# Kernel tuning notes

Measured on AMD Instinct MI355X. Metric: run time of the kernel, lower is better.

Reference implementation:

```python
import jax, jax.numpy as jnp
import numpy as np

VOCAB_SIZE = 148
START_IDX = 1
LATENT = 32
HID = 256
NUM_LAYERS = 2
B = 8192
T = 50


def setup_inputs() -> dict:
    key = jax.random.key(0)
    ks = jax.random.split(key, 20)
    s = 0.05
    inp = {
        "z": jax.random.normal(ks[0], (B, LATENT), jnp.float32),
        "target_tokens": jax.random.randint(ks[1], (B, T), 0, VOCAB_SIZE),
        "emb": jax.random.normal(ks[2], (VOCAB_SIZE, HID), jnp.float32) * s,
        "W_lat": jax.random.normal(ks[3], (HID * NUM_LAYERS, LATENT), jnp.float32) * s,
        "b_lat": jnp.zeros((HID * NUM_LAYERS,), jnp.float32),
        "W_ih0": jax.random.normal(ks[4], (3 * HID, HID), jnp.float32) * s,
        "W_hh0": jax.random.normal(ks[5], (3 * HID, HID), jnp.float32) * s,
        "b_ih0": jnp.zeros((3 * HID,), jnp.float32),
        "b_hh0": jnp.zeros((3 * HID,), jnp.float32),
        "W_ih1": jax.random.normal(ks[6], (3 * HID, HID), jnp.float32) * s,
        "W_hh1": jax.random.normal(ks[7], (3 * HID, HID), jnp.float32) * s,
        "b_ih1": jnp.zeros((3 * HID,), jnp.float32),
        "b_hh1": jnp.zeros((3 * HID,), jnp.float32),
        "W1": jax.random.normal(ks[8], (HID, HID), jnp.float32) * s,
        "b1": jnp.zeros((HID,), jnp.float32),
        "W2": jax.random.normal(ks[9], (VOCAB_SIZE, HID), jnp.float32) * s,
        "b2": jnp.zeros((VOCAB_SIZE,), jnp.float32),
    }
    # padding_idx=0 row of embedding is zero in torch
    inp["emb"] = inp["emb"].at[0].set(0.0)
    return inp


def _gru_cell(x, h, W_ih, W_hh, b_ih, b_hh):
    # PyTorch GRUCell math
    gi = x @ W_ih.T + b_ih          # [B, 3H]
    gh = h @ W_hh.T + b_hh          # [B, 3H]
    i_r, i_z, i_n = jnp.split(gi, 3, axis=-1)
    h_r, h_z, h_n = jnp.split(gh, 3, axis=-1)
    r = jax.nn.sigmoid(i_r + h_r)
    zg = jax.nn.sigmoid(i_z + h_z)
    n = jnp.tanh(i_n + r * h_n)
    return (1.0 - zg) * n + zg * h


def reference(z, target_tokens, emb, W_lat, b_lat,
              W_ih0, W_hh0, b_ih0, b_hh0,
              W_ih1, W_hh1, b_ih1, b_hh1,
              W1, b1, W2, b2):
    batch = z.shape[0]
    # init hidden: (B, L*H) -> (L, B, H)
    h = (z @ W_lat.T + b_lat).reshape(batch, NUM_LAYERS, HID).transpose(1, 0, 2)
    # teacher forcing ratio 1.0: inputs = [START, tgt[:,1], ..., tgt[:,T-2]]
    start = jnp.full((batch, 1), START_IDX, dtype=target_tokens.dtype)
    tokens_in = jnp.concatenate([start, target_tokens[:, 1:T - 1]], axis=1)  # [B, T-1]
    x = emb[tokens_in]                       # [B, T-1, H]
    xs = x.transpose(1, 0, 2)                # [T-1, B, H]

    def step(carry, x_t):
        h0, h1 = carry
        h0n = _gru_cell(x_t, h0, W_ih0, W_hh0, b_ih0, b_hh0)
        h1n = _gru_cell(h0n, h1, W_ih1, W_hh1, b_ih1, b_hh1)
        return (h0n, h1n), h1n

    _, ys = jax.lax.scan(step, (h[0], h[1]), xs)   # ys: [T-1, B, H]
    y = ys.transpose(1, 0, 2)                      # [B, T-1, H]
    hdd = jax.nn.relu(jnp.einsum('bth,oh->bto', y, W1) + b1)
    logits = jnp.einsum('bth,vh->btv', hdd, W2) + b2   # [B, T-1, V]
    generated = target_tokens[:, 1:]                   # pure teacher forcing
    return logits, generated
```

## Files before the change

kernel.cpp:

```cpp
#include <hip/hip_runtime.h>
#include <hip/hip_bf16.h>
#include <math.h>


#define BATCH 8192
#define TTOT 50
#define TS 49
#define HID 256
#define N3 768
#define VOCAB 148
#define START_TOK 1
#define HPAD 264

typedef short bf16x8 __attribute__((ext_vector_type(8)));
typedef float f32x4 __attribute__((ext_vector_type(4)));

constexpr size_t OFF_Y    = 0;
constexpr size_t OFF_WH0B = OFF_Y + 205520896;
constexpr size_t OFF_WI1B = OFF_WH0B + 393216;
constexpr size_t OFF_WH1B = OFF_WI1B + 393216;
constexpr size_t OFF_W1B  = OFF_WH1B + 393216;
constexpr size_t OFF_W2B  = OFF_W1B + 131072;
constexpr size_t OFF_TAB  = OFF_W2B + 81920;
constexpr size_t OFF_H0F  = OFF_TAB + 454656;
constexpr size_t OFF_H1F  = OFF_H0F + 8388608;

__device__ __forceinline__ short f2b(float f) {
    union { float f; unsigned int u; } v; v.f = f;
    unsigned int u = v.u;
    return (short)((u + 0x7FFFu + ((u >> 16) & 1u)) >> 16);
}
__device__ __forceinline__ float sigm(float x) {
    x = fminf(fmaxf(x, -30.f), 30.f);
    return 1.f / (1.f + __expf(-x));
}
__device__ __forceinline__ float tanh_(float x) {
    x = fminf(fmaxf(x, -15.f), 15.f);
    float e = __expf(-2.f * x);
    return (1.f - e) / (1.f + e);
}

__global__ __launch_bounds__(256) void convert_w(
    const float* __restrict__ Wh0, const float* __restrict__ Wi1, const float* __restrict__ Wh1,
    const float* __restrict__ W1, const float* __restrict__ W2,
    short* __restrict__ Wh0b, short* __restrict__ Wi1b, short* __restrict__ Wh1b,
    short* __restrict__ W1b, short* __restrict__ W2b)
{
    int tid = blockIdx.x * 256 + threadIdx.x;
    const int WSZ = N3 * HID;
    const float* S; short* D; int n; bool pad148 = false;
    if (tid < WSZ) { S = Wh0; D = Wh0b; n = tid; }
    else if (tid < 2 * WSZ) { S = Wi1; D = Wi1b; n = tid - WSZ; }
    else if (tid < 3 * WSZ) { S = Wh1; D = Wh1b; n = tid - 2 * WSZ; }
    else if (tid < 3 * WSZ + 65536) { S = W1; D = W1b; n = tid - 3 * WSZ; }
    else if (tid < 3 * WSZ + 65536 + 40960) { S = W2; D = W2b; n = tid - 3 * WSZ - 65536; pad148 = true; }
    else return;
    int e = n & 7, lane = (n >> 3) & 63, kc = (n >> 9) & 7, nt = n >> 12;
    int row = nt * 16 + (lane & 15);
    int k = kc * 32 + (lane >> 4) * 8 + e;
    float v = (pad148 && row >= VOCAB) ? 0.f : S[row * HID + k];
    D[n] = f2b(v);
}

__global__ __launch_bounds__(256) void build_tab(
    const float* __restrict__ emb, const float* __restrict__ Wih0,
    const float* __restrict__ bih0, float* __restrict__ tab)
{
    int o = blockIdx.x * 256 + threadIdx.x;
    if (o >= VOCAB * N3) return;
    int v = o / N3, c = o - v * N3;
    const float* er = emb + v * HID;
    const float* wr = Wih0 + c * HID;
    float s = bih0[c];
    #pragma unroll 8
    for (int k = 0; k < HID; ++k) s += er[k] * wr[k];
    tab[o] = s;
}

__global__ __launch_bounds__(256) void init_h(
    const float* __restrict__ z, const float* __restrict__ Wl, const float* __restrict__ bl,
    float* __restrict__ h0f, float* __restrict__ h1f)
{
    int tid = blockIdx.x * 256 + threadIdx.x;
    int b = tid >> 9, o = tid & 511;
    const float* zr = z + b * 32;
    const float* wr = Wl + o * 32;
    float s = bl[o];
    #pragma unroll
    for (int k = 0; k < 32; ++k) s += zr[k] * wr[k];
    if (o < HID) h0f[b * HID + o] = s;
    else         h1f[b * HID + o - HID] = s;
}

__global__ __launch_bounds__(512, 2) void gru_persistent(
    const int* __restrict__ toks, const float* __restrict__ tab,
    const short* __restrict__ Wh0, const short* __restrict__ Wi1, const short* __restrict__ Wh1,
    const float* __restrict__ bhh0, const float* __restrict__ bih1, const float* __restrict__ bhh1,
    const float* __restrict__ h0f, const float* __restrict__ h1f,
    short* __restrict__ Yb)
{
    __shared__ short h0L[32 * HPAD];
    __shared__ short h1L[32 * HPAD];
    __shared__ int tokL[32 * TTOT];

    const int tid = threadIdx.x;
    const int wave = tid >> 6, lane = tid & 63, quad = lane >> 4, l15 = lane & 15;
    const int rowbase = blockIdx.x * 32;

    for (int idx = tid; idx < 1024; idx += 512) {
        int row = idx >> 5, col = (idx & 31) * 8;
        const float* s0 = h0f + (size_t)(rowbase + row) * HID + col;
        const float* s1 = h1f + (size_t)(rowbase + row) * HID + col;
        short t0[8], t1[8];
        #pragma unroll
        for (int j = 0; j < 8; ++j) { t0[j] = f2b(s0[j]); t1[j] = f2b(s1[j]); }
        *(bf16x8*)&h0L[row * HPAD + col] = *(bf16x8*)t0;
        *(bf16x8*)&h1L[row * HPAD + col] = *(bf16x8*)t1;
    }
    for (int idx = tid; idx < 32 * TTOT; idx += 512) {
        int row = idx / TTOT, tt = idx - row * TTOT;
        tokL[idx] = (tt == 0) ? START_TOK : toks[(size_t)(rowbase + row) * TTOT + tt];
    }

    float h0r[2][2][4], h1r[2][2][4];
    #pragma unroll
    for (int i = 0; i < 2; ++i)
        #pragma unroll
        for (int c = 0; c < 2; ++c) {
            int col = wave * 32 + c * 16 + l15;
            #pragma unroll
            for (int r_ = 0; r_ < 4; ++r_) {
                int row = rowbase + 16 * i + quad * 4 + r_;
                h0r[i][c][r_] = h0f[(size_t)row * HID + col];
                h1r[i][c][r_] = h1f[(size_t)row * HID + col];
            }
        }
    __syncthreads();

    const short* WA[6]; const short* WB[6]; const short* WC[6];
    #pragma unroll
    for (int g = 0; g < 3; ++g)
        #pragma unroll
        for (int c = 0; c < 2; ++c) {
            int nt = g * 16 + wave * 2 + c;
            WA[g * 2 + c] = Wh0 + (size_t)nt * 4096 + lane * 8;
            WB[g * 2 + c] = Wh1 + (size_t)nt * 4096 + lane * 8;
            WC[g * 2 + c] = Wi1 + (size_t)nt * 4096 + lane * 8;
        }

    const size_t mtg0 = (size_t)(rowbase >> 4);

    for (int t = 0; t < TS; ++t) {
        f32x4 acc0[2][6] = {};
        f32x4 accrz[2][4] = {}, acchn[2][2] = {};
        #pragma unroll 2
        for (int kc = 0; kc < 8; ++kc) {
            bf16x8 a0[2], a1[2];
            #pragma unroll
            for (int i = 0; i < 2; ++i) {
                a0[i] = *(const bf16x8*)&h0L[(16 * i + l15) * HPAD + kc * 32 + quad * 8];
                a1[i] = *(const bf16x8*)&h1L[(16 * i + l15) * HPAD + kc * 32 + quad * 8];
            }
            #pragma unroll
            for (int j = 0; j < 6; ++j) {
                bf16x8 b0 = *(const bf16x8*)(WA[j] + kc * 512);
                #pragma unroll
                for (int i = 0; i < 2; ++i)
                    acc0[i][j] = __builtin_amdgcn_mfma_f32_16x16x32_bf16(a0[i], b0, acc0[i][j], 0, 0, 0);
            }
            #pragma unroll
            for (int j = 0; j < 6; ++j) {
                bf16x8 b1 = *(const bf16x8*)(WB[j] + kc * 512);
                #pragma unroll
                for (int i = 0; i < 2; ++i) {
                    if (j < 4) accrz[i][j] = __builtin_amdgcn_mfma_f32_16x16x32_bf16(a1[i], b1, accrz[i][j], 0, 0, 0);
                    else       acchn[i][j - 4] = __builtin_amdgcn_mfma_f32_16x16x32_bf16(a1[i], b1, acchn[i][j - 4], 0, 0, 0);
                }
            }
        }
        #pragma unroll
        for (int c = 0; c < 2; ++c) {
            int col = wave * 32 + c * 16 + l15;
            float br = bhh0[col], bz = bhh0[256 + col], bn = bhh0[512 + col];
            #pragma unroll
            for (int i = 0; i < 2; ++i)
                #pragma unroll
                for (int r_ = 0; r_ < 4; ++r_) {
                    int rl = 16 * i + quad * 4 + r_;
                    const float* tp = tab + (size_t)tokL[rl * TTOT + t] * N3 + col;
                    float r  = sigm(acc0[i][c][r_] + br + tp[0]);
                    float z  = sigm(acc0[i][2 + c][r_] + bz + tp[256]);
                    float n  = tanh_(tp[512] + r * (acc0[i][4 + c][r_] + bn));
                    h0r[i][c][r_] = (1.f - z) * n + z * h0r[i][c][r_];
                }
        }
        __syncthreads();
        #pragma unroll
        for (int c = 0; c < 2; ++c) {
            int col = wave * 32 + c * 16 + l15;
            #pragma unroll
            for (int i = 0; i < 2; ++i)
                #pragma unroll
                for (int r_ = 0; r_ < 4; ++r_)
                    h0L[(16 * i + quad * 4 + r_) * HPAD + col] = f2b(h0r[i][c][r_]);
        }
        __syncthreads();

        f32x4 accgn[2][2] = {};
        #pragma unroll 2
        for (int kc = 0; kc < 8; ++kc) {
            bf16x8 a[2];
            #pragma unroll
            for (int i = 0; i < 2; ++i)
                a[i] = *(const bf16x8*)&h0L[(16 * i + l15) * HPAD + kc * 32 + quad * 8];
            #pragma unroll
            for (int j = 0; j < 6; ++j) {
                bf16x8 b = *(const bf16x8*)(WC[j] + kc * 512);
                #pragma unroll
                for (int i = 0; i < 2; ++i) {
                    if (j < 4) accrz[i][j] = __builtin_amdgcn_mfma_f32_16x16x32_bf16(a[i], b, accrz[i][j], 0, 0, 0);
                    else       accgn[i][j - 4] = __builtin_amdgcn_mfma_f32_16x16x32_bf16(a[i], b, accgn[i][j - 4], 0, 0, 0);
                }
            }
        }
        #pragma unroll
        for (int c = 0; c < 2; ++c) {
            int col = wave * 32 + c * 16 + l15;
            float brr = bih1[col] + bhh1[col];
            float brz = bih1[256 + col] + bhh1[256 + col];
            float bni = bih1[512 + col], bnh = bhh1[512 + col];
            #pragma unroll
            for (int i = 0; i < 2; ++i)
                #pragma unroll
                for (int r_ = 0; r_ < 4; ++r_) {
                    float r = sigm(accrz[i][c][r_] + brr);
                    float z = sigm(accrz[i][2 + c][r_] + brz);
                    float n = tanh_(accgn[i][c][r_] + bni + r * (acchn[i][c][r_] + bnh));
                    h1r[i][c][r_] = (1.f - z) * n + z * h1r[i][c][r_];
                }
        }
        __syncthreads();
        #pragma unroll
        for (int c = 0; c < 2; ++c) {
            int col = wave * 32 + c * 16 + l15;
            #pragma unroll
            for (int i = 0; i < 2; ++i)
                #pragma unroll
                for (int r_ = 0; r_ < 4; ++r_)
                    h1L[(16 * i + quad * 4 + r_) * HPAD + col] = f2b(h1r[i][c][r_]);
        }
        __syncthreads();

        #pragma unroll
        for (int it = 0; it < 2; ++it) {
            int pair = wave + it * 8;
            int mt = pair >> 3, kc = pair & 7;
            bf16x8 v = *(const bf16x8*)&h1L[(mt * 16 + l15) * HPAD + kc * 32 + quad * 8];
            *(bf16x8*)(Yb + ((((size_t)t * 512 + mtg0 + mt) * 8 + kc) << 9) + lane * 8) = v;
        }
    }
}

__global__ __launch_bounds__(256) void head_kernel(
    const short* __restrict__ YP, const short* __restrict__ W1P, const float* __restrict__ b1,
    const short* __restrict__ W2P, const float* __restrict__ b2, float* __restrict__ out)
{
    __shared__ short hddL[64 * HPAD];
    int wave = threadIdx.x >> 6;
    int lane = threadIdx.x & 63;
    int quad = lane >> 4;
    int l15  = lane & 15;
    int rbase = blockIdx.x * 64;
    int tt = rbase >> 13;
    int mb = (rbase & 8191) >> 4;

    {
        const short* ybase = YP + ((size_t)tt * 512 + mb) * 4096 + lane * 8;
        const short* wbase = W1P + (size_t)(wave * 4) * 4096 + lane * 8;
        f32x4 acc[4][4] = {};
        #pragma unroll 2
        for (int kc = 0; kc < 8; ++kc) {
            bf16x8 a[4], bfr[4];
            #pragma unroll
            for (int i = 0; i < 4; ++i) a[i] = *(const bf16x8*)(ybase + (size_t)i * 4096 + kc * 512);
            #pragma unroll
            for (int j = 0; j < 4; ++j) bfr[j] = *(const bf16x8*)(wbase + (size_t)j * 4096 + kc * 512);
            #pragma unroll
            for (int i = 0; i < 4; ++i)
                #pragma unroll
                for (int j = 0; j < 4; ++j)
                    acc[i][j] = __builtin_amdgcn_mfma_f32_16x16x32_bf16(a[i], bfr[j], acc[i][j], 0, 0, 0);
        }
        #pragma unroll
        for (int i = 0; i < 4; ++i)
            #pragma unroll
            for (int j = 0; j < 4; ++j)
                #pragma unroll
                for (int r = 0; r < 4; ++r) {
                    int rl = i * 16 + quad * 4 + r;
                    int c  = wave * 64 + j * 16 + l15;
                    float v = acc[i][j][r] + b1[c];
                    hddL[rl * HPAD + c] = f2b(fmaxf(v, 0.f));
                }
    }
    __syncthreads();
    for (int s = wave * 5; s < wave * 5 + 5; ++s) {
        int ct = s >> 1, rh = s & 1;
        const short* w2b = W2P + (size_t)ct * 4096 + lane * 8;
        f32x4 acc2[2] = {};
        #pragma unroll 2
        for (int kc = 0; kc < 8; ++kc) {
            bf16x8 bfr = *(const bf16x8*)(w2b + kc * 512);
            #pragma unroll
            for (int it = 0; it < 2; ++it) {
                bf16x8 a = *(const bf16x8*)&hddL[(rh * 32 + it * 16 + l15) * HPAD + kc * 32 + quad * 8];
                acc2[it] = __builtin_amdgcn_mfma_f32_16x16x32_bf16(a, bfr, acc2[it], 0, 0, 0);
            }
        }
        int col = ct * 16 + l15;
        if (col < VOCAB) {
            #pragma unroll
            for (int it = 0; it < 2; ++it)
                #pragma unroll
                for (int r = 0; r < 4; ++r) {
                    int rl = rh * 32 + it * 16 + quad * 4 + r;
                    int gr = rbase + rl;
                    int t2 = gr >> 13;
                    int bb = gr & 8191;
                    out[((size_t)bb * TS + t2) * VOCAB + col] = acc2[it][r] + b2[col];
                }
        }
    }
}

__global__ __launch_bounds__(256) void gen_copy(const int* __restrict__ toks, float* __restrict__ out2)
{
    int tid = blockIdx.x * 256 + threadIdx.x;
    if (tid < BATCH * TS) {
        int b = tid / TS, j = tid - b * TS;
        out2[tid] = (float)toks[b * TTOT + j + 1];
    }
}

extern "C" void kernel_launch(void* const* d_in, const int* in_sizes, int n_in,
                              void* d_out, int out_size, void* d_ws, size_t ws_size,
                              hipStream_t stream) {
    const float* z     = (const float*)d_in[0];
    const int*   toks  = (const int*)d_in[1];
    const float* emb   = (const float*)d_in[2];
    const float* W_lat = (const float*)d_in[3];
    const float* b_lat = (const float*)d_in[4];
    const float* W_ih0 = (const float*)d_in[5];
    const float* W_hh0 = (const float*)d_in[6];
    const float* b_ih0 = (const float*)d_in[7];
    const float* b_hh0 = (const float*)d_in[8];
    const float* W_ih1 = (const float*)d_in[9];
    const float* W_hh1 = (const float*)d_in[10];
    const float* b_ih1 = (const float*)d_in[11];
    const float* b_hh1 = (const float*)d_in[12];
    const float* W1    = (const float*)d_in[13];
    const float* b1    = (const float*)d_in[14];
    const float* W2    = (const float*)d_in[15];
    const float* b2    = (const float*)d_in[16];

    char* w = (char*)d_ws;
    short* Yb   = (short*)(w + OFF_Y);
    short* Wh0b = (short*)(w + OFF_WH0B);
    short* Wi1b = (short*)(w + OFF_WI1B);
    short* Wh1b = (short*)(w + OFF_WH1B);
    short* W1b  = (short*)(w + OFF_W1B);
    short* W2b  = (short*)(w + OFF_W2B);
    float* tab  = (float*)(w + OFF_TAB);
    float* h0f  = (float*)(w + OFF_H0F);
    float* h1f  = (float*)(w + OFF_H1F);

    float* out_logits = (float*)d_out;
    float* out_gen    = out_logits + (size_t)BATCH * TS * VOCAB;

    convert_w<<<2720, 256, 0, stream>>>(W_hh0, W_ih1, W_hh1, W1, W2,
                                        Wh0b, Wi1b, Wh1b, W1b, W2b);
    build_tab<<<(VOCAB * N3 + 255) / 256, 256, 0, stream>>>(emb, W_ih0, b_ih0, tab);
    init_h<<<(BATCH * 512) / 256, 256, 0, stream>>>(z, W_lat, b_lat, h0f, h1f);
    gen_copy<<<(BATCH * TS + 255) / 256, 256, 0, stream>>>(toks, out_gen);

    gru_persistent<<<256, 512, 0, stream>>>(toks, tab, Wh0b, Wi1b, Wh1b,
                                            b_hh0, b_ih1, b_hh1, h0f, h1f, Yb);

    head_kernel<<<(BATCH * TS) / 64, 256, 0, stream>>>(Yb, W1b, b1, W2b, b2, out_logits);
}
```

Measured before the change: 1.440 ms.

## Halve GRU rows per block, double grid, fold biases into split input tables

The persistent GRU kernel now gives each block 16 batch rows instead of 32 and launches 512 blocks with higher occupancy bounds, so more blocks and CUs share the serial recurrence. The layer-0 input table is split into an interleaved r/z table, with the hidden biases folded in, and a separate n table, so the gate loads are paired float2 reads. Biases are hoisted out of the time loop, sigmoid clamps are removed, and bf16 packing uses v_cvt_pk_bf16_f32. Trade-off: each block reuses every weight fragment it loads across half as many rows, so total weight traffic from L2 roughly doubles.

```diff
diff --git a/kernel.cpp b/kernel.cpp
--- a/kernel.cpp
+++ b/kernel.cpp
@@ -22,6 +22,7 @@
 constexpr size_t OFF_W1B  = OFF_WH1B + 393216;
 constexpr size_t OFF_W2B  = OFF_W1B + 131072;
 constexpr size_t OFF_TAB  = OFF_W2B + 81920;
+constexpr size_t OFF_TABN = OFF_TAB + 303104;
 constexpr size_t OFF_H0F  = OFF_TAB + 454656;
 constexpr size_t OFF_H1F  = OFF_H0F + 8388608;
 
@@ -31,11 +32,10 @@
     return (short)((u + 0x7FFFu + ((u >> 16) & 1u)) >> 16);
 }
 __device__ __forceinline__ float sigm(float x) {
-    x = fminf(fmaxf(x, -30.f), 30.f);
     return 1.f / (1.f + __expf(-x));
 }
 __device__ __forceinline__ float tanh_(float x) {
-    x = fminf(fmaxf(x, -15.f), 15.f);
+    x = fmaxf(x, -15.f);
     float e = __expf(-2.f * x);
     return (1.f - e) / (1.f + e);
 }
@@ -62,19 +62,23 @@
     D[n] = f2b(v);
 }
 
-__global__ __launch_bounds__(256) void build_tab(
+__global__ __launch_bounds__(256) void build_tab2(
     const float* __restrict__ emb, const float* __restrict__ Wih0,
-    const float* __restrict__ bih0, float* __restrict__ tab)
+    const float* __restrict__ bih0, const float* __restrict__ bhh0,
+    float* __restrict__ tab_rz, float* __restrict__ tab_n)
 {
     int o = blockIdx.x * 256 + threadIdx.x;
     if (o >= VOCAB * N3) return;
-    int v = o / N3, c = o - v * N3;
+    int v = o / N3, cc = o - v * N3;
+    int g = cc >> 8, c = cc & 255;
     const float* er = emb + v * HID;
-    const float* wr = Wih0 + c * HID;
-    float s = bih0[c];
+    const float* wr = Wih0 + cc * HID;
+    float s = bih0[cc];
     #pragma unroll 8
     for (int k = 0; k < HID; ++k) s += er[k] * wr[k];
-    tab[o] = s;
+    if (g == 0)      tab_rz[(((v << 8) + c) << 1) + 0] = s + bhh0[c];
+    else if (g == 1) tab_rz[(((v << 8) + c) << 1) + 1] = s + bhh0[256 + c];
+    else             tab_n[(v << 8) + c] = s;
 }
 
 __global__ __launch_bounds__(256) void init_h(
@@ -92,23 +96,24 @@
     else         h1f[b * HID + o - HID] = s;
 }
 
-__global__ __launch_bounds__(512, 2) void gru_persistent(
-    const int* __restrict__ toks, const float* __restrict__ tab,
+__global__ __launch_bounds__(512, 4) void gru_persistent(
+    const int* __restrict__ toks,
+    const float* __restrict__ tab_rz, const float* __restrict__ tab_n,
     const short* __restrict__ Wh0, const short* __restrict__ Wi1, const short* __restrict__ Wh1,
     const float* __restrict__ bhh0, const float* __restrict__ bih1, const float* __restrict__ bhh1,
     const float* __restrict__ h0f, const float* __restrict__ h1f,
     short* __restrict__ Yb)
 {
-    __shared__ short h0L[32 * HPAD];
-    __shared__ short h1L[32 * HPAD];
-    __shared__ int tokL[32 * TTOT];
+    __shared__ short h0L[16 * HPAD];
+    __shared__ short h1L[16 * HPAD];
+    __shared__ int tokL[16 * TTOT];
 
     const int tid = threadIdx.x;
     const int wave = tid >> 6, lane = tid & 63, quad = lane >> 4, l15 = lane & 15;
-    const int rowbase = blockIdx.x * 32;
-
-    for (int idx = tid; idx < 1024; idx += 512) {
-        int row = idx >> 5, col = (idx & 31) * 8;
+    const int rowbase = blockIdx.x * 16;
+
+    {
+        int row = tid >> 5, col = (tid & 31) * 8;
         const float* s0 = h0f + (size_t)(rowbase + row) * HID + col;
         const float* s1 = h1f + (size_t)(rowbase + row) * HID + col;
         short t0[8], t1[8];
@@ -117,147 +122,131 @@
         *(bf16x8*)&h0L[row * HPAD + col] = *(bf16x8*)t0;
         *(bf16x8*)&h1L[row * HPAD + col] = *(bf16x8*)t1;
     }
-    for (int idx = tid; idx < 32 * TTOT; idx += 512) {
+    for (int idx = tid; idx < 16 * TTOT; idx += 512) {
         int row = idx / TTOT, tt = idx - row * TTOT;
         tokL[idx] = (tt == 0) ? START_TOK : toks[(size_t)(rowbase + row) * TTOT + tt];
     }
 
-    float h0r[2][2][4], h1r[2][2][4];
-    #pragma unroll
-    for (int i = 0; i < 2; ++i)
-        #pragma unroll
-        for (int c = 0; c < 2; ++c) {
-            int col = wave * 32 + c * 16 + l15;
-            #pragma unroll
-            for (int r_ = 0; r_ < 4; ++r_) {
-                int row = rowbase + 16 * i + quad * 4 + r_;
-                h0r[i][c][r_] = h0f[(size_t)row * HID + col];
-                h1r[i][c][r_] = h1f[(size_t)row * HID + col];
-            }
-        }
+    int colc[2]; colc[0] = wave * 32 + l15; colc[1] = colc[0] + 16;
+    float h0r[2][4], h1r[2][4];
+    #pragma unroll
+    for (int c = 0; c < 2; ++c)
+        #pragma unroll
+        for (int r_ = 0; r_ < 4; ++r_) {
+            int row = rowbase + quad * 4 + r_;
+            h0r[c][r_] = h0f[(size_t)row * HID + colc[c]];
+            h1r[c][r_] = h1f[(size_t)row * HID + colc[c]];
+        }
+
+    float bn0[2], brr[2], brz[2], bni[2], bnh[2];
+    #pragma unroll
+    for (int c = 0; c < 2; ++c) {
+        int col = colc[c];
+        bn0[c] = bhh0[512 + col];
+        brr[c] = bih1[col] + bhh1[col];
+        brz[c] = bih1[256 + col] + bhh1[256 + col];
+        bni[c] = bih1[512 + col];
+        bnh[c] = bhh1[512 + col];
+    }
+
+    int woff[6];
+    #pragma unroll
+    for (int g = 0; g < 3; ++g)
+        #pragma unroll
+        for (int c = 0; c < 2; ++c)
+            woff[g * 2 + c] = ((g * 16 + wave * 2 + c) << 12) + lane * 8;
+
+    const int a0base = l15 * HPAD + quad * 8;
+    const int hwbase = (quad * 4) * HPAD + colc[0];
+    int tokrow[4];
+    #pragma unroll
+    for (int r_ = 0; r_ < 4; ++r_) tokrow[r_] = (quad * 4 + r_) * TTOT;
+    short* yptr = Yb + ((((size_t)blockIdx.x << 3) + wave) << 9) + lane * 8;
+
     __syncthreads();
 
-    const short* WA[6]; const short* WB[6]; const short* WC[6];
-    #pragma unroll
-    for (int g = 0; g < 3; ++g)
-        #pragma unroll
-        for (int c = 0; c < 2; ++c) {
-            int nt = g * 16 + wave * 2 + c;
-            WA[g * 2 + c] = Wh0 + (size_t)nt * 4096 + lane * 8;
-            WB[g * 2 + c] = Wh1 + (size_t)nt * 4096 + lane * 8;
-            WC[g * 2 + c] = Wi1 + (size_t)nt * 4096 + lane * 8;
-        }
-
-    const size_t mtg0 = (size_t)(rowbase >> 4);
-
     for (int t = 0; t < TS; ++t) {
-        f32x4 acc0[2][6] = {};
-        f32x4 accrz[2][4] = {}, acchn[2][2] = {};
+        f32x4 acc0[6] = {};
+        f32x4 accrz[4] = {}, acchn[2] = {};
         #pragma unroll 2
         for (int kc = 0; kc < 8; ++kc) {
-            bf16x8 a0[2], a1[2];
-            #pragma unroll
-            for (int i = 0; i < 2; ++i) {
-                a0[i] = *(const bf16x8*)&h0L[(16 * i + l15) * HPAD + kc * 32 + quad * 8];
-                a1[i] = *(const bf16x8*)&h1L[(16 * i + l15) * HPAD + kc * 32 + quad * 8];
-            }
+            bf16x8 a0 = *(const bf16x8*)&h0L[a0base + kc * 32];
+            bf16x8 a1 = *(const bf16x8*)&h1L[a0base + kc * 32];
             #pragma unroll
             for (int j = 0; j < 6; ++j) {
-                bf16x8 b0 = *(const bf16x8*)(WA[j] + kc * 512);
-                #pragma unroll
-                for (int i = 0; i < 2; ++i)
-                    acc0[i][j] = __builtin_amdgcn_mfma_f32_16x16x32_bf16(a0[i], b0, acc0[i][j], 0, 0, 0);
+                bf16x8 b0 = *(const bf16x8*)(Wh0 + woff[j] + kc * 512);
+                acc0[j] = __builtin_amdgcn_mfma_f32_16x16x32_bf16(a0, b0, acc0[j], 0, 0, 0);
             }
             #pragma unroll
             for (int j = 0; j < 6; ++j) {
-                bf16x8 b1 = *(const bf16x8*)(WB[j] + kc * 512);
-                #pragma unroll
-                for (int i = 0; i < 2; ++i) {
-                    if (j < 4) accrz[i][j] = __builtin_amdgcn_mfma_f32_16x16x32_bf16(a1[i], b1, accrz[i][j], 0, 0, 0);
-                    else       acchn[i][j - 4] = __builtin_amdgcn_mfma_f32_16x16x32_bf16(a1[i], b1, acchn[i][j - 4], 0, 0, 0);
-                }
-            }
-        }
-        #pragma unroll
-        for (int c = 0; c < 2; ++c) {
-            int col = wave * 32 + c * 16 + l15;
-            float br = bhh0[col], bz = bhh0[256 + col], bn = bhh0[512 + col];
-            #pragma unroll
-            for (int i = 0; i < 2; ++i)
-                #pragma unroll
-                for (int r_ = 0; r_ < 4; ++r_) {
-                    int rl = 16 * i + quad * 4 + r_;
-                    const float* tp = tab + (size_t)tokL[rl * TTOT + t] * N3 + col;
-                    float r  = sigm(acc0[i][c][r_] + br + tp[0]);
-                    float z  = sigm(acc0[i][2 + c][r_] + bz + tp[256]);
-                    float n  = tanh_(tp[512] + r * (acc0[i][4 + c][r_] + bn));
-                    h0r[i][c][r_] = (1.f - z) * n + z * h0r[i][c][r_];
-                }
+                bf16x8 b1 = *(const bf16x8*)(Wh1 + woff[j] + kc * 512);
+                if (j < 4) accrz[j] = __builtin_amdgcn_mfma_f32_16x16x32_bf16(a1, b1, accrz[j], 0, 0, 0);
+                else       acchn[j - 4] = __builtin_amdgcn_mfma_f32_16x16x32_bf16(a1, b1, acchn[j - 4], 0, 0, 0);
+            }
+        }
+        #pragma unroll
+        for (int r_ = 0; r_ < 4; ++r_) {
+            int tok = tokL[tokrow[r_] + t];
+            const float2 rz0 = *(const float2*)(tab_rz + (tok << 9) + (colc[0] << 1));
+            const float2 rz1 = *(const float2*)(tab_rz + (tok << 9) + (colc[1] << 1));
+            float in0 = tab_n[(tok << 8) + colc[0]];
+            float in1 = tab_n[(tok << 8) + colc[1]];
+            {
+                float r = sigm(acc0[0][r_] + rz0.x);
+                float z = sigm(acc0[2][r_] + rz0.y);
+                float n = tanh_(in0 + r * (acc0[4][r_] + bn0[0]));
+                h0r[0][r_] = n + z * (h0r[0][r_] - n);
+            }
+            {
+                float r = sigm(acc0[1][r_] + rz1.x);
+                float z = sigm(acc0[3][r_] + rz1.y);
+                float n = tanh_(in1 + r * (acc0[5][r_] + bn0[1]));
+                h0r[1][r_] = n + z * (h0r[1][r_] - n);
+            }
         }
         __syncthreads();
         #pragma unroll
-        for (int c = 0; c < 2; ++c) {
-            int col = wave * 32 + c * 16 + l15;
-            #pragma unroll
-            for (int i = 0; i < 2; ++i)
-                #pragma unroll
-                for (int r_ = 0; r_ < 4; ++r_)
-                    h0L[(16 * i + quad * 4 + r_) * HPAD + col] = f2b(h0r[i][c][r_]);
+        for (int r_ = 0; r_ < 4; ++r_) {
+            unsigned u;
+            asm("v_cvt_pk_bf16_f32 %0, %1, %2" : "=v"(u) : "v"(h0r[0][r_]), "v"(h0r[1][r_]));
+            int ro = hwbase + r_ * HPAD;
+            h0L[ro]      = (short)u;
+            h0L[ro + 16] = (short)(u >> 16);
         }
         __syncthreads();
 
-        f32x4 accgn[2][2] = {};
+        f32x4 accgn[2] = {};
         #pragma unroll 2
         for (int kc = 0; kc < 8; ++kc) {
-            bf16x8 a[2];
-            #pragma unroll
-            for (int i = 0; i < 2; ++i)
-                a[i] = *(const bf16x8*)&h0L[(16 * i + l15) * HPAD + kc * 32 + quad * 8];
+            bf16x8 a = *(const bf16x8*)&h0L[a0base + kc * 32];
             #pragma unroll
             for (int j = 0; j < 6; ++j) {
-                bf16x8 b = *(const bf16x8*)(WC[j] + kc * 512);
-                #pragma unroll
-                for (int i = 0; i < 2; ++i) {
-                    if (j < 4) accrz[i][j] = __builtin_amdgcn_mfma_f32_16x16x32_bf16(a[i], b, accrz[i][j], 0, 0, 0);
-                    else       accgn[i][j - 4] = __builtin_amdgcn_mfma_f32_16x16x32_bf16(a[i], b, accgn[i][j - 4], 0, 0, 0);
-                }
-            }
-        }
-        #pragma unroll
-        for (int c = 0; c < 2; ++c) {
-            int col = wave * 32 + c * 16 + l15;
-            float brr = bih1[col] + bhh1[col];
-            float brz = bih1[256 + col] + bhh1[256 + col];
-            float bni = bih1[512 + col], bnh = bhh1[512 + col];
-            #pragma unroll
-            for (int i = 0; i < 2; ++i)
-                #pragma unroll
-                for (int r_ = 0; r_ < 4; ++r_) {
-                    float r = sigm(accrz[i][c][r_] + brr);
-                    float z = sigm(accrz[i][2 + c][r_] + brz);
-                    float n = tanh_(accgn[i][c][r_] + bni + r * (acchn[i][c][r_] + bnh));
-                    h1r[i][c][r_] = (1.f - z) * n + z * h1r[i][c][r_];
-                }
+                bf16x8 b = *(const bf16x8*)(Wi1 + woff[j] + kc * 512);
+                if (j < 4) accrz[j] = __builtin_amdgcn_mfma_f32_16x16x32_bf16(a, b, accrz[j], 0, 0, 0);
+                else       accgn[j - 4] = __builtin_amdgcn_mfma_f32_16x16x32_bf16(a, b, accgn[j - 4], 0, 0, 0);
+            }
+        }
+        #pragma unroll
+        for (int c = 0; c < 2; ++c)
+            #pragma unroll
+            for (int r_ = 0; r_ < 4; ++r_) {
+                float r = sigm(accrz[c][r_] + brr[c]);
+                float z = sigm(accrz[2 + c][r_] + brz[c]);
+                float n = tanh_(accgn[c][r_] + bni[c] + r * (acchn[c][r_] + bnh[c]));
+                h1r[c][r_] = n + z * (h1r[c][r_] - n);
+            }
+        #pragma unroll
+        for (int r_ = 0; r_ < 4; ++r_) {
+            unsigned u;
+            asm("v_cvt_pk_bf16_f32 %0, %1, %2" : "=v"(u) : "v"(h1r[0][r_]), "v"(h1r[1][r_]));
+            int ro = hwbase + r_ * HPAD;
+            h1L[ro]      = (short)u;
+            h1L[ro + 16] = (short)(u >> 16);
         }
         __syncthreads();
-        #pragma unroll
-        for (int c = 0; c < 2; ++c) {
-            int col = wave * 32 + c * 16 + l15;
-            #pragma unroll
-            for (int i = 0; i < 2; ++i)
-                #pragma unroll
-                for (int r_ = 0; r_ < 4; ++r_)
-                    h1L[(16 * i + quad * 4 + r_) * HPAD + col] = f2b(h1r[i][c][r_]);
-        }
-        __syncthreads();
-
-        #pragma unroll
-        for (int it = 0; it < 2; ++it) {
-            int pair = wave + it * 8;
-            int mt = pair >> 3, kc = pair & 7;
-            bf16x8 v = *(const bf16x8*)&h1L[(mt * 16 + l15) * HPAD + kc * 32 + quad * 8];
-            *(bf16x8*)(Yb + ((((size_t)t * 512 + mtg0 + mt) * 8 + kc) << 9) + lane * 8) = v;
-        }
+
+        *(bf16x8*)yptr = *(const bf16x8*)&h1L[a0base + wave * 32];
+        yptr += (size_t)512 * 8 * 512;
     }
 }
 
@@ -364,26 +353,27 @@
     const float* b2    = (const float*)d_in[16];
 
     char* w = (char*)d_ws;
-    short* Yb   = (short*)(w + OFF_Y);
-    short* Wh0b = (short*)(w + OFF_WH0B);
-    short* Wi1b = (short*)(w + OFF_WI1B);
-    short* Wh1b = (short*)(w + OFF_WH1B);
-    short* W1b  = (short*)(w + OFF_W1B);
-    short* W2b  = (short*)(w + OFF_W2B);
-    float* tab  = (float*)(w + OFF_TAB);
-    float* h0f  = (float*)(w + OFF_H0F);
-    float* h1f  = (float*)(w + OFF_H1F);
+    short* Yb    = (short*)(w + OFF_Y);
+    short* Wh0b  = (short*)(w + OFF_WH0B);
+    short* Wi1b  = (short*)(w + OFF_WI1B);
+    short* Wh1b  = (short*)(w + OFF_WH1B);
+    short* W1b   = (short*)(w + OFF_W1B);
+    short* W2b   = (short*)(w + OFF_W2B);
+    float* tabrz = (float*)(w + OFF_TAB);
+    float* tabn  = (float*)(w + OFF_TABN);
+    float* h0f   = (float*)(w + OFF_H0F);
+    float* h1f   = (float*)(w + OFF_H1F);
 
     float* out_logits = (float*)d_out;
     float* out_gen    = out_logits + (size_t)BATCH * TS * VOCAB;
 
     convert_w<<<2720, 256, 0, stream>>>(W_hh0, W_ih1, W_hh1, W1, W2,
                                         Wh0b, Wi1b, Wh1b, W1b, W2b);
-    build_tab<<<(VOCAB * N3 + 255) / 256, 256, 0, stream>>>(emb, W_ih0, b_ih0, tab);
+    build_tab2<<<(VOCAB * N3 + 255) / 256, 256, 0, stream>>>(emb, W_ih0, b_ih0, b_hh0, tabrz, tabn);
     init_h<<<(BATCH * 512) / 256, 256, 0, stream>>>(z, W_lat, b_lat, h0f, h1f);
     gen_copy<<<(BATCH * TS + 255) / 256, 256, 0, stream>>>(toks, out_gen);
 
-    gru_persistent<<<256, 512, 0, stream>>>(toks, tab, Wh0b, Wi1b, Wh1b,
+    gru_persistent<<<512, 512, 0, stream>>>(toks, tabrz, tabn, Wh0b, Wi1b, Wh1b,
                                             b_hh0, b_ih1, b_hh1, h0f, h1f, Yb);
 
     head_kernel<<<(BATCH * TS) / 64, 256, 0, stream>>>(Yb, W1b, b1, W2b, b2, out_logits);
```

After: 2.596 ms. +80.3%, slower.
